# Optimization experiments

Hardware: AMD Instinct MI355X
Metric: run time of the kernel (lower is better)

## Reference

```python
import jax, jax.numpy as jnp
import numpy as np

TEMPERATURE = 30.0
K = 4  # num_kernels


def setup_inputs() -> dict:
    key = jax.random.key(0)
    ks = jax.random.split(key, 8)
    B, H, W_, Cin = 32, 128, 128, 64
    F, kh, kw = 64, 3, 3
    hidden = Cin // 4  # attention_reduction_ratio = 4
    # glorot-uniform-ish scales
    def glorot(k, shape, fan_in, fan_out):
        lim = np.sqrt(6.0 / (fan_in + fan_out)).astype(np.float32)
        return jax.random.uniform(k, shape, jnp.float32, -lim, lim)
    x = jax.random.normal(ks[0], (B, H, W_, Cin), jnp.float32)
    # K parallel conv kernels [K, kh, kw, Cin, F] (HWIO per kernel)
    Wk = glorot(ks[1], (K, kh, kw, Cin, F), kh * kw * Cin, kh * kw * F)
    bk = jnp.zeros((K, F), jnp.float32)
    att_w1 = glorot(ks[2], (Cin, hidden), Cin, hidden)
    att_b1 = jnp.zeros((hidden,), jnp.float32)
    att_w2 = glorot(ks[3], (hidden, K), hidden, K)
    att_b2 = jnp.zeros((K,), jnp.float32)
    return {"x": x, "Wk": Wk, "bk": bk, "att_w1": att_w1, "att_b1": att_b1,
            "att_w2": att_w2, "att_b2": att_b2}


def _dynamic_conv(x, Wk, bk, att_w1, att_b1, att_w2, att_b2):
    # Attention over kernels: GAP -> MLP -> softmax(logits / tau)
    pooled = jnp.mean(x, axis=(1, 2))                      # [B, Cin]
    h = jax.nn.relu(pooled @ att_w1 + att_b1)              # [B, hidden]
    logits = h @ att_w2 + att_b2                           # [B, K]
    pi = jax.nn.softmax(logits / TEMPERATURE, axis=-1)     # [B, K]
    # Weight-space aggregation: per-sample kernel, then single conv per sample.
    # Mathematically equal to sum_k pi_k * conv(x, W_k) since conv is linear in W.
    W_agg = jnp.einsum('bk,khwio->bhwio', pi, Wk)          # [B, kh, kw, Cin, F]
    b_agg = pi @ bk                                        # [B, F]

    def conv_one(xi, wi):
        # xi: [H, W, Cin], wi: [kh, kw, Cin, F]
        return jax.lax.conv_general_dilated(
            xi[None], wi, window_strides=(1, 1), padding='SAME',
            dimension_numbers=('NHWC', 'HWIO', 'NHWC'))[0]

    y = jax.vmap(conv_one)(x, W_agg)                       # [B, H, W, F]
    return y + b_agg[:, None, None, :]


def reference(x, Wk, bk, att_w1, att_b1, att_w2, att_b2):
    return _dynamic_conv(x, Wk, bk, att_w1, att_b1, att_w2, att_b2)
```

## Files before the change

### kernel.cpp

```cpp
#include <hip/hip_runtime.h>
#include <hip/hip_bf16.h>
#include <stdint.h>

typedef __bf16 bf16x8 __attribute__((ext_vector_type(8)));
typedef float f32x4 __attribute__((ext_vector_type(4)));

#define XS_BYTES 46080

__device__ __forceinline__ void load_lds16(const void* gsrc, void* ldst) {
    __builtin_amdgcn_global_load_lds(
        (const __attribute__((address_space(1))) uint32_t*)gsrc,
        (__attribute__((address_space(3))) uint32_t*)ldst, 16, 0, 0);
}

__global__ void pool_kernel(const float* __restrict__ x, float* __restrict__ pooled) {
    __shared__ float red[64];
    const int tid = threadIdx.x;
    if (tid < 64) red[tid] = 0.f;
    __syncthreads();
    const int b = blockIdx.x >> 6;
    const float4* x4 = reinterpret_cast<const float4*>(x) + (long)blockIdx.x * 4096;
    float4 s = {0.f, 0.f, 0.f, 0.f};
    #pragma unroll
    for (int i = 0; i < 16; ++i) {
        float4 v = x4[tid + 256 * i];
        s.x += v.x; s.y += v.y; s.z += v.z; s.w += v.w;
    }
    const int c0 = (tid & 15) * 4;
    atomicAdd(&red[c0 + 0], s.x);
    atomicAdd(&red[c0 + 1], s.y);
    atomicAdd(&red[c0 + 2], s.z);
    atomicAdd(&red[c0 + 3], s.w);
    __syncthreads();
    if (tid < 64) atomicAdd(&pooled[b * 64 + tid], red[tid]);
}

__global__ __launch_bounds__(256)
void wagg_kernel(const float* __restrict__ pooled, const float* __restrict__ Wk,
                 const float* __restrict__ bk,
                 const float* __restrict__ w1, const float* __restrict__ b1,
                 const float* __restrict__ w2, const float* __restrict__ b2,
                 __hip_bfloat16* __restrict__ Wt, float* __restrict__ bagg) {
    const int b = blockIdx.x, j = blockIdx.y, tid = threadIdx.x;
    __shared__ float accs[64][64];
    __shared__ float hsh[16], lg[4], pish[4];

    const int f4 = (tid & 15) * 4;
    const int kr = tid >> 4;
    float4 v[4][4];
    #pragma unroll
    for (int pass = 0; pass < 4; ++pass) {
        const int k = j * 64 + pass * 16 + kr;
        #pragma unroll
        for (int kk = 0; kk < 4; ++kk)
            v[pass][kk] = *reinterpret_cast<const float4*>(Wk + (size_t)kk * 36864 + k * 64 + f4);
    }
    if (tid < 16) {
        float a = 0.f;
        for (int c = 0; c < 64; ++c)
            a += pooled[b * 64 + c] * (1.f / 16384.f) * w1[c * 16 + tid];
        hsh[tid] = fmaxf(a + b1[tid], 0.f);
    }
    __syncthreads();
    if (tid < 4) {
        float a = 0.f;
        for (int jj = 0; jj < 16; ++jj) a += hsh[jj] * w2[jj * 4 + tid];
        lg[tid] = (a + b2[tid]) * (1.f / 30.f);
    }
    __syncthreads();
    if (tid == 0) {
        float m = fmaxf(fmaxf(lg[0], lg[1]), fmaxf(lg[2], lg[3]));
        float e0 = expf(lg[0] - m), e1 = expf(lg[1] - m), e2 = expf(lg[2] - m), e3 = expf(lg[3] - m);
        float inv = 1.f / (e0 + e1 + e2 + e3);
        pish[0] = e0 * inv; pish[1] = e1 * inv; pish[2] = e2 * inv; pish[3] = e3 * inv;
    }
    __syncthreads();
    const float p0 = pish[0], p1 = pish[1], p2 = pish[2], p3 = pish[3];
    #pragma unroll
    for (int pass = 0; pass < 4; ++pass) {
        float4 a;
        a.x = p0*v[pass][0].x + p1*v[pass][1].x + p2*v[pass][2].x + p3*v[pass][3].x;
        a.y = p0*v[pass][0].y + p1*v[pass][1].y + p2*v[pass][2].y + p3*v[pass][3].y;
        a.z = p0*v[pass][0].z + p1*v[pass][1].z + p2*v[pass][2].z + p3*v[pass][3].z;
        a.w = p0*v[pass][0].w + p1*v[pass][1].w + p2*v[pass][2].w + p3*v[pass][3].w;
        *reinterpret_cast<float4*>(&accs[pass * 16 + kr][f4]) = a;
    }
    __syncthreads();
    const int f = tid & 63;
    const int kgo0 = (tid >> 6) * 2;
    #pragma unroll
    for (int t2 = 0; t2 < 2; ++t2) {
        const int kgo = kgo0 + t2;
        bf16x8 o;
        #pragma unroll
        for (int i = 0; i < 8; ++i) o[i] = (__bf16)accs[kgo * 8 + i][f];
        *reinterpret_cast<bf16x8*>(Wt + (size_t)b * 36864 + f * 576 + (j * 8 + kgo) * 8) = o;
    }
    if (j == 0 && tid < 64)
        bagg[b * 64 + tid] = p0*bk[tid] + p1*bk[64+tid] + p2*bk[128+tid] + p3*bk[192+tid];
}

__global__ __launch_bounds__(256, 1)
void conv_kernel(const float* __restrict__ x, const __hip_bfloat16* __restrict__ Wt,
                 const float* __restrict__ bagg, const float* __restrict__ zeros,
                 float* __restrict__ out) {
    extern __shared__ char smem[];
    const int tid = threadIdx.x;
    const int b  = blockIdx.x >> 3;
    const int th = blockIdx.x & 7;
    const int lane = tid & 63;
    const int wv  = tid >> 6;
    const int l15 = lane & 15;
    const int q   = lane >> 4;

    bf16x8 Bf[4][18];
    {
        const __hip_bfloat16* Wb = Wt + (size_t)b * 36864;
        #pragma unroll
        for (int nf = 0; nf < 4; ++nf) {
            const __hip_bfloat16* fp = Wb + (nf * 16 + l15) * 576 + q * 8;
            #pragma unroll
            for (int s = 0; s < 18; ++s)
                Bf[nf][s] = *reinterpret_cast<const bf16x8*>(fp + s * 32);
        }
    }
    float bagg_v[4];
    #pragma unroll
    for (int nf = 0; nf < 4; ++nf) bagg_v[nf] = bagg[b * 64 + nf * 16 + l15];

    const size_t xb = (size_t)b * (128 * 128 * 64);
    const int h0 = th * 16 - 1;
    const int wave_g0 = tid & 192;

    auto stage = [&](int buf, int tw) {
        const int w0 = tw * 8 - 1;
        char* bufb = smem + buf * XS_BYTES;
        #pragma unroll
        for (int i = 0; i < 12; ++i) {
            const int g = i * 256 + tid;
            if (g < 2880) {
                const int r  = g / 160;
                const int u  = g - r * 160;
                const int p  = u >> 4;
                const int cg = u & 15;
                const int gh = h0 + r, gw = w0 + p;
                const int scg = cg ^ (p & 7);
                const float* src = ((unsigned)gh < 128u && (unsigned)gw < 128u)
                    ? x + xb + (size_t)(gh * 128 + gw) * 64 + scg * 4
                    : zeros + scg * 4;
                load_lds16(src, bufb + ((i * 256 + wave_g0) << 4));
            }
        }
    };

    stage(0, 0);
    __syncthreads();

    #pragma unroll 1
    for (int tw = 0; tw < 16; ++tw) {
        if (tw < 15) stage((tw + 1) & 1, tw + 1);
        const char* bufb = smem + (tw & 1) * XS_BYTES;

        f32x4 acc[2][4];
        #pragma unroll
        for (int mf = 0; mf < 2; ++mf)
            #pragma unroll
            for (int nf = 0; nf < 4; ++nf) acc[mf][nf] = (f32x4){0.f, 0.f, 0.f, 0.f};

        #pragma unroll
        for (int s = 0; s < 18; ++s) {
            const int tap = s >> 1;
            const int dh  = tap / 3;
            const int dw  = tap - dh * 3;
            const int cg0 = (s & 1) * 8 + q * 2;
            #pragma unroll
            for (int mf = 0; mf < 2; ++mf) {
                const int r = wv * 4 + mf * 2 + (l15 >> 3) + dh;
                const int c = (l15 & 7) + dw;
                const int gbase = (r * 160 + c * 16 + cg0) << 4;
                const int sw = (c & 7) << 4;
                const f32x4 x0 = *reinterpret_cast<const f32x4*>(bufb + (gbase ^ sw));
                const f32x4 x1 = *reinterpret_cast<const f32x4*>(bufb + ((gbase + 16) ^ sw));
                bf16x8 af;
                af[0] = (__bf16)x0[0]; af[1] = (__bf16)x0[1];
                af[2] = (__bf16)x0[2]; af[3] = (__bf16)x0[3];
                af[4] = (__bf16)x1[0]; af[5] = (__bf16)x1[1];
                af[6] = (__bf16)x1[2]; af[7] = (__bf16)x1[3];
                #pragma unroll
                for (int nf = 0; nf < 4; ++nf)
                    acc[mf][nf] = __builtin_amdgcn_mfma_f32_16x16x32_bf16(af, Bf[nf][s], acc[mf][nf], 0, 0, 0);
            }
        }

        #pragma unroll
        for (int mf = 0; mf < 2; ++mf) {
            #pragma unroll
            for (int jj = 0; jj < 4; ++jj) {
                const int P  = wv * 32 + mf * 16 + q * 4 + jj;
                const int hh = th * 16 + (P >> 3);
                const int ww = tw * 8 + (P & 7);
                float* op = out + ((size_t)b * 16384 + hh * 128 + ww) * 64 + l15;
                #pragma unroll
                for (int nf = 0; nf < 4; ++nf)
                    op[nf * 16] = acc[mf][nf][jj] + bagg_v[nf];
            }
        }
        __syncthreads();
    }
}

extern "C" void kernel_launch(void* const* d_in, const int* in_sizes, int n_in,
                              void* d_out, int out_size, void* d_ws, size_t ws_size,
                              hipStream_t stream) {
    const float* x   = (const float*)d_in[0];
    const float* Wk  = (const float*)d_in[1];
    const float* bk  = (const float*)d_in[2];
    const float* w1  = (const float*)d_in[3];
    const float* b1  = (const float*)d_in[4];
    const float* w2  = (const float*)d_in[5];
    const float* b2  = (const float*)d_in[6];
    float* out = (float*)d_out;

    char* ws = (char*)d_ws;
    float* pooled = (float*)ws;
    float* bagg   = (float*)(ws + 8192);
    float* zeros  = (float*)(ws + 16384);
    __hip_bfloat16* Wt = (__hip_bfloat16*)(ws + 20480);

    hipMemsetAsync(pooled, 0, 8192, stream);
    hipMemsetAsync(zeros, 0, 4096, stream);
    pool_kernel<<<2048, 256, 0, stream>>>(x, pooled);
    wagg_kernel<<<dim3(32, 9), 256, 0, stream>>>(pooled, Wk, bk, w1, b1, w2, b2, Wt, bagg);

    static bool attr_set = false;
    if (!attr_set) {
        hipFuncSetAttribute((const void*)conv_kernel,
                            hipFuncAttributeMaxDynamicSharedMemorySize, 2 * XS_BYTES);
        attr_set = true;
    }
    conv_kernel<<<256, 256, 2 * XS_BYTES, stream>>>(x, Wt, bagg, zeros, out);
}
```

Baseline: 317.1 us.

## Stage input as bf16 in LDS via registers, widen conv tiles, drop atomics and memsets

The conv kernel now stages input tiles through registers and converts them to bf16 before writing to LDS. This halves the LDS footprint and removes the per-tap fp32-to-bf16 conversion in the inner loop. Tiles grow to 16x16 pixels, and the block now has 512 threads with waves split across M and N. The next tile is loaded in two halves interleaved with the MFMA steps to overlap global loads with compute. The pooling kernel writes per-block partial sums that wagg_kernel reduces, replacing the global atomics and memsets; the catch is higher register pressure and more store code in the loop.

```diff
diff --git a/kernel.cpp b/kernel.cpp
--- a/kernel.cpp
+++ b/kernel.cpp
@@ -5,24 +5,17 @@
 typedef __bf16 bf16x8 __attribute__((ext_vector_type(8)));
 typedef float f32x4 __attribute__((ext_vector_type(4)));
 
-#define XS_BYTES 46080
-
-__device__ __forceinline__ void load_lds16(const void* gsrc, void* ldst) {
-    __builtin_amdgcn_global_load_lds(
-        (const __attribute__((address_space(1))) uint32_t*)gsrc,
-        (__attribute__((address_space(3))) uint32_t*)ldst, 16, 0, 0);
-}
-
-__global__ void pool_kernel(const float* __restrict__ x, float* __restrict__ pooled) {
+#define XS_BYTES 41472
+
+__global__ void pool_kernel(const float* __restrict__ x, float* __restrict__ part) {
     __shared__ float red[64];
     const int tid = threadIdx.x;
     if (tid < 64) red[tid] = 0.f;
     __syncthreads();
-    const int b = blockIdx.x >> 6;
-    const float4* x4 = reinterpret_cast<const float4*>(x) + (long)blockIdx.x * 4096;
+    const float4* x4 = reinterpret_cast<const float4*>(x) + (size_t)blockIdx.x * 8192;
     float4 s = {0.f, 0.f, 0.f, 0.f};
     #pragma unroll
-    for (int i = 0; i < 16; ++i) {
+    for (int i = 0; i < 32; ++i) {
         float4 v = x4[tid + 256 * i];
         s.x += v.x; s.y += v.y; s.z += v.z; s.w += v.w;
     }
@@ -32,18 +25,19 @@
     atomicAdd(&red[c0 + 2], s.z);
     atomicAdd(&red[c0 + 3], s.w);
     __syncthreads();
-    if (tid < 64) atomicAdd(&pooled[b * 64 + tid], red[tid]);
+    if (tid < 64) part[(size_t)blockIdx.x * 64 + tid] = red[tid];
 }
 
 __global__ __launch_bounds__(256)
-void wagg_kernel(const float* __restrict__ pooled, const float* __restrict__ Wk,
+void wagg_kernel(const float* __restrict__ part, const float* __restrict__ Wk,
                  const float* __restrict__ bk,
                  const float* __restrict__ w1, const float* __restrict__ b1,
                  const float* __restrict__ w2, const float* __restrict__ b2,
                  __hip_bfloat16* __restrict__ Wt, float* __restrict__ bagg) {
     const int b = blockIdx.x, j = blockIdx.y, tid = threadIdx.x;
     __shared__ float accs[64][64];
-    __shared__ float hsh[16], lg[4], pish[4];
+    __shared__ float psum[4][64];
+    __shared__ float pool_sh[64], hsh[16], lg[4], pish[4];
 
     const int f4 = (tid & 15) * 4;
     const int kr = tid >> 4;
@@ -55,10 +49,20 @@
         for (int kk = 0; kk < 4; ++kk)
             v[pass][kk] = *reinterpret_cast<const float4*>(Wk + (size_t)kk * 36864 + k * 64 + f4);
     }
+    {
+        const int c = tid & 63, qq = tid >> 6;
+        float s = 0.f;
+        #pragma unroll
+        for (int r = 0; r < 8; ++r) s += part[((size_t)b * 32 + qq * 8 + r) * 64 + c];
+        psum[qq][c] = s;
+    }
+    __syncthreads();
+    if (tid < 64)
+        pool_sh[tid] = (psum[0][tid] + psum[1][tid] + psum[2][tid] + psum[3][tid]) * (1.f / 16384.f);
+    __syncthreads();
     if (tid < 16) {
         float a = 0.f;
-        for (int c = 0; c < 64; ++c)
-            a += pooled[b * 64 + c] * (1.f / 16384.f) * w1[c * 16 + tid];
+        for (int c = 0; c < 64; ++c) a += pool_sh[c] * w1[c * 16 + tid];
         hsh[tid] = fmaxf(a + b1[tid], 0.f);
     }
     __syncthreads();
@@ -100,112 +104,139 @@
         bagg[b * 64 + tid] = p0*bk[tid] + p1*bk[64+tid] + p2*bk[128+tid] + p3*bk[192+tid];
 }
 
-__global__ __launch_bounds__(256, 1)
+
+template<int S>
+__device__ __forceinline__ void cstep(const char* bufb, int wm, int l15, int q,
+                                      const bf16x8 (&Bf)[2][18], f32x4 (&acc)[4][2]) {
+    constexpr int tap = S >> 1, half = S & 1;
+    constexpr int dh = tap / 3, dw = tap % 3;
+    #pragma unroll
+    for (int mf = 0; mf < 4; ++mf) {
+        const int r = wm * 4 + mf + dh;
+        const int c = l15 + dw;
+        const int pix = r * 18 + c;
+        const int off = ((pix * 8 + half * 4 + q) << 4) ^ ((pix & 7) << 4);
+        const bf16x8 af = *reinterpret_cast<const bf16x8*>(bufb + off);
+        acc[mf][0] = __builtin_amdgcn_mfma_f32_16x16x32_bf16(af, Bf[0][S], acc[mf][0], 0, 0, 0);
+        acc[mf][1] = __builtin_amdgcn_mfma_f32_16x16x32_bf16(af, Bf[1][S], acc[mf][1], 0, 0, 0);
+    }
+}
+
+template<int S0, int S1>
+__device__ __forceinline__ void crange(const char* bufb, int wm, int l15, int q,
+                                       const bf16x8 (&Bf)[2][18], f32x4 (&acc)[4][2]) {
+    if constexpr (S0 < S1) {
+        cstep<S0>(bufb, wm, l15, q, Bf, acc);
+        crange<S0 + 1, S1>(bufb, wm, l15, q, Bf, acc);
+    }
+}
+
+__global__ __launch_bounds__(512, 2)
 void conv_kernel(const float* __restrict__ x, const __hip_bfloat16* __restrict__ Wt,
-                 const float* __restrict__ bagg, const float* __restrict__ zeros,
-                 float* __restrict__ out) {
+                 const float* __restrict__ bagg, float* __restrict__ out) {
     extern __shared__ char smem[];
-    const int tid = threadIdx.x;
-    const int b  = blockIdx.x >> 3;
-    const int th = blockIdx.x & 7;
+    const int tid  = threadIdx.x;
+    const int b    = blockIdx.x >> 3;
+    const int th   = blockIdx.x & 7;
     const int lane = tid & 63;
-    const int wv  = tid >> 6;
-    const int l15 = lane & 15;
-    const int q   = lane >> 4;
-
-    bf16x8 Bf[4][18];
+    const int w    = tid >> 6;
+    const int wm   = w >> 1;
+    const int wn   = w & 1;
+    const int l15  = lane & 15;
+    const int q    = lane >> 4;
+
+    bf16x8 Bf[2][18];
     {
         const __hip_bfloat16* Wb = Wt + (size_t)b * 36864;
         #pragma unroll
-        for (int nf = 0; nf < 4; ++nf) {
-            const __hip_bfloat16* fp = Wb + (nf * 16 + l15) * 576 + q * 8;
+        for (int nf = 0; nf < 2; ++nf) {
+            const __hip_bfloat16* fp = Wb + (wn * 32 + nf * 16 + l15) * 576 + q * 8;
             #pragma unroll
             for (int s = 0; s < 18; ++s)
                 Bf[nf][s] = *reinterpret_cast<const bf16x8*>(fp + s * 32);
         }
     }
-    float bagg_v[4];
-    #pragma unroll
-    for (int nf = 0; nf < 4; ++nf) bagg_v[nf] = bagg[b * 64 + nf * 16 + l15];
+    float bagg_v[2];
+    #pragma unroll
+    for (int nf = 0; nf < 2; ++nf) bagg_v[nf] = bagg[b * 64 + wn * 32 + nf * 16 + l15];
 
     const size_t xb = (size_t)b * (128 * 128 * 64);
     const int h0 = th * 16 - 1;
-    const int wave_g0 = tid & 192;
-
-    auto stage = [&](int buf, int tw) {
-        const int w0 = tw * 8 - 1;
+
+    float4 svA[3][2], svB[3][2];
+
+    auto sload = [&](int tw, float4 (&sv)[3][2], int i0) {
+        const int w0 = tw * 16 - 1;
+        #pragma unroll
+        for (int i = 0; i < 3; ++i) {
+            const int g = (i0 + i) * 512 + tid;
+            float4 va = {0.f,0.f,0.f,0.f}, vb = {0.f,0.f,0.f,0.f};
+            if (g < 2592) {
+                const int pix = g >> 3;
+                const int r = pix / 18;
+                const int c = pix - r * 18;
+                const int gh = h0 + r, gw = w0 + c;
+                if ((unsigned)gh < 128u && (unsigned)gw < 128u) {
+                    const float* src = x + xb + ((size_t)(gh * 128 + gw) * 64 + (g & 7) * 8);
+                    va = *reinterpret_cast<const float4*>(src);
+                    vb = *reinterpret_cast<const float4*>(src + 4);
+                }
+            }
+            sv[i][0] = va; sv[i][1] = vb;
+        }
+    };
+    auto swrite = [&](int buf, float4 (&sv)[3][2], int i0) {
         char* bufb = smem + buf * XS_BYTES;
         #pragma unroll
-        for (int i = 0; i < 12; ++i) {
-            const int g = i * 256 + tid;
-            if (g < 2880) {
-                const int r  = g / 160;
-                const int u  = g - r * 160;
-                const int p  = u >> 4;
-                const int cg = u & 15;
-                const int gh = h0 + r, gw = w0 + p;
-                const int scg = cg ^ (p & 7);
-                const float* src = ((unsigned)gh < 128u && (unsigned)gw < 128u)
-                    ? x + xb + (size_t)(gh * 128 + gw) * 64 + scg * 4
-                    : zeros + scg * 4;
-                load_lds16(src, bufb + ((i * 256 + wave_g0) << 4));
+        for (int i = 0; i < 3; ++i) {
+            const int g = (i0 + i) * 512 + tid;
+            if (g < 2592) {
+                bf16x8 o;
+                o[0] = (__bf16)sv[i][0].x; o[1] = (__bf16)sv[i][0].y;
+                o[2] = (__bf16)sv[i][0].z; o[3] = (__bf16)sv[i][0].w;
+                o[4] = (__bf16)sv[i][1].x; o[5] = (__bf16)sv[i][1].y;
+                o[6] = (__bf16)sv[i][1].z; o[7] = (__bf16)sv[i][1].w;
+                const int off = (g << 4) ^ (((g >> 3) & 7) << 4);
+                *reinterpret_cast<bf16x8*>(bufb + off) = o;
             }
         }
     };
 
-    stage(0, 0);
-    __syncthreads();
+    sload(0, svA, 0);
+    sload(0, svB, 3);
+    swrite(0, svA, 0);
+    swrite(0, svB, 3);
 
     #pragma unroll 1
-    for (int tw = 0; tw < 16; ++tw) {
-        if (tw < 15) stage((tw + 1) & 1, tw + 1);
+    for (int tw = 0; tw < 8; ++tw) {
+        __syncthreads();
         const char* bufb = smem + (tw & 1) * XS_BYTES;
-
-        f32x4 acc[2][4];
-        #pragma unroll
-        for (int mf = 0; mf < 2; ++mf)
+        const int nxt = (tw + 1) & 1;
+
+        f32x4 acc[4][2];
+        #pragma unroll
+        for (int mf = 0; mf < 4; ++mf) {
+            acc[mf][0] = (f32x4){0.f, 0.f, 0.f, 0.f};
+            acc[mf][1] = (f32x4){0.f, 0.f, 0.f, 0.f};
+        }
+
+        if (tw < 7) sload(tw + 1, svA, 0);
+        crange<0, 9>(bufb, wm, l15, q, Bf, acc);
+        if (tw < 7) { swrite(nxt, svA, 0); sload(tw + 1, svB, 3); }
+        crange<9, 18>(bufb, wm, l15, q, Bf, acc);
+        if (tw < 7) swrite(nxt, svB, 3);
+
+        #pragma unroll
+        for (int mf = 0; mf < 4; ++mf) {
+            const int hh = th * 16 + wm * 4 + mf;
+            float* rowp = out + (((size_t)b * 128 + hh) * 128 + tw * 16) * 64 + wn * 32 + l15;
             #pragma unroll
-            for (int nf = 0; nf < 4; ++nf) acc[mf][nf] = (f32x4){0.f, 0.f, 0.f, 0.f};
-
-        #pragma unroll
-        for (int s = 0; s < 18; ++s) {
-            const int tap = s >> 1;
-            const int dh  = tap / 3;
-            const int dw  = tap - dh * 3;
-            const int cg0 = (s & 1) * 8 + q * 2;
-            #pragma unroll
-            for (int mf = 0; mf < 2; ++mf) {
-                const int r = wv * 4 + mf * 2 + (l15 >> 3) + dh;
-                const int c = (l15 & 7) + dw;
-                const int gbase = (r * 160 + c * 16 + cg0) << 4;
-                const int sw = (c & 7) << 4;
-                const f32x4 x0 = *reinterpret_cast<const f32x4*>(bufb + (gbase ^ sw));
-                const f32x4 x1 = *reinterpret_cast<const f32x4*>(bufb + ((gbase + 16) ^ sw));
-                bf16x8 af;
-                af[0] = (__bf16)x0[0]; af[1] = (__bf16)x0[1];
-                af[2] = (__bf16)x0[2]; af[3] = (__bf16)x0[3];
-                af[4] = (__bf16)x1[0]; af[5] = (__bf16)x1[1];
-                af[6] = (__bf16)x1[2]; af[7] = (__bf16)x1[3];
-                #pragma unroll
-                for (int nf = 0; nf < 4; ++nf)
-                    acc[mf][nf] = __builtin_amdgcn_mfma_f32_16x16x32_bf16(af, Bf[nf][s], acc[mf][nf], 0, 0, 0);
+            for (int j = 0; j < 4; ++j) {
+                const int ww = q * 4 + j;
+                rowp[(size_t)ww * 64]      = acc[mf][0][j] + bagg_v[0];
+                rowp[(size_t)ww * 64 + 16] = acc[mf][1][j] + bagg_v[1];
             }
         }
-
-        #pragma unroll
-        for (int mf = 0; mf < 2; ++mf) {
-            #pragma unroll
-            for (int jj = 0; jj < 4; ++jj) {
-                const int P  = wv * 32 + mf * 16 + q * 4 + jj;
-                const int hh = th * 16 + (P >> 3);
-                const int ww = tw * 8 + (P & 7);
-                float* op = out + ((size_t)b * 16384 + hh * 128 + ww) * 64 + l15;
-                #pragma unroll
-                for (int nf = 0; nf < 4; ++nf)
-                    op[nf * 16] = acc[mf][nf][jj] + bagg_v[nf];
-            }
-        }
-        __syncthreads();
     }
 }
 
@@ -222,15 +253,12 @@
     float* out = (float*)d_out;
 
     char* ws = (char*)d_ws;
-    float* pooled = (float*)ws;
-    float* bagg   = (float*)(ws + 8192);
-    float* zeros  = (float*)(ws + 16384);
-    __hip_bfloat16* Wt = (__hip_bfloat16*)(ws + 20480);
-
-    hipMemsetAsync(pooled, 0, 8192, stream);
-    hipMemsetAsync(zeros, 0, 4096, stream);
-    pool_kernel<<<2048, 256, 0, stream>>>(x, pooled);
-    wagg_kernel<<<dim3(32, 9), 256, 0, stream>>>(pooled, Wk, bk, w1, b1, w2, b2, Wt, bagg);
+    float* part = (float*)ws;
+    float* bagg = (float*)(ws + 262144);
+    __hip_bfloat16* Wt = (__hip_bfloat16*)(ws + 270336);
+
+    pool_kernel<<<1024, 256, 0, stream>>>(x, part);
+    wagg_kernel<<<dim3(32, 9), 256, 0, stream>>>(part, Wk, bk, w1, b1, w2, b2, Wt, bagg);
 
     static bool attr_set = false;
     if (!attr_set) {
@@ -238,5 +266,5 @@
                             hipFuncAttributeMaxDynamicSharedMemorySize, 2 * XS_BYTES);
         attr_set = true;
     }
-    conv_kernel<<<256, 256, 2 * XS_BYTES, stream>>>(x, Wt, bagg, zeros, out);
-}
+    conv_kernel<<<256, 512, 2 * XS_BYTES, stream>>>(x, Wt, bagg, out);
+}
```

Result: slower. 462.0 us (+45.7%).
